# Kernel tuning notes

Hardware: AMD Instinct MI355X
Metric: run time of the kernel (lower is better)

Reference implementation:

```python
import jax, jax.numpy as jnp
import numpy as np

EPS = 1e-8
ALPHA = 0.5


def _min_max_normalize(y):
    y_min = jnp.min(y)
    y_max = jnp.max(y)
    return (y - y_min) / (y_max - y_min + EPS)


def setup_inputs() -> dict:
    key = jax.random.key(0)
    k1, k2, k3, k4 = jax.random.split(key, 4)
    nr, nb, d = 8, 2048, 32
    n_train = 8192
    x = jax.random.uniform(k1, (nr, nb, d), dtype=jnp.float32)
    train_x = jax.random.uniform(k2, (n_train, d), dtype=jnp.float32)
    train_residuals = jax.random.uniform(k3, (n_train,), dtype=jnp.float32)
    sigma_x = jax.random.uniform(k4, (nr, nb), dtype=jnp.float32)
    return {"x": x, "train_x": train_x,
            "train_residuals": train_residuals, "sigma_x": sigma_x}


def reference(x, train_x, train_residuals, sigma_x):
    nr, nb, d = x.shape
    n = train_x.shape[0]

    # Scott's rule bandwidth: mean(std(X, dim=0)) * n^(-1/(d+4)); torch std is unbiased
    std_devs = jnp.std(train_x, axis=0, ddof=1)
    bandwidth = jnp.mean(std_devs) * (float(n) ** (-1.0 / (d + 4)))
    inv_bw_sq = 1.0 / (2.0 * bandwidth * bandwidth)

    # KDE residual estimate (Nadaraya-Watson): cdist^2 -> exp -> weighted sum
    xq = x.reshape(nr * nb, d)                     # [m, d]
    d2 = (jnp.sum(xq * xq, axis=1)[:, None]
          + jnp.sum(train_x * train_x, axis=1)[None, :]
          - 2.0 * (xq @ train_x.T))                # [m, n]
    d2 = jnp.maximum(d2, 0.0)
    kernel_weights = jnp.exp(-d2 * inv_bw_sq)      # [m, n]
    rx = (kernel_weights @ train_residuals) / (jnp.sum(kernel_weights, axis=1) + EPS)

    T1 = ALPHA * _min_max_normalize(rx).reshape(nr, nb)
    T2 = (1.0 - ALPHA) * _min_max_normalize(sigma_x.reshape(-1)).reshape(nr, nb)
    return T1 + T2
```

## Files before the change

kernel.cpp:

```cpp
#include <hip/hip_runtime.h>
#include <math.h>

#define EPSF 1e-8f
#define LOG2E 1.44269504f

typedef short short8 __attribute__((ext_vector_type(8)));
typedef float floatx4 __attribute__((ext_vector_type(4)));

__device__ __forceinline__ unsigned short f2bf(float f) {
    unsigned u = __builtin_bit_cast(unsigned, f);
    unsigned r = (u + 0x7FFFu + ((u >> 16) & 1u)) >> 16;
    return (unsigned short)r;
}
__device__ __forceinline__ float bf2f(unsigned short h) {
    return __builtin_bit_cast(float, ((unsigned)h) << 16);
}

__global__ __launch_bounds__(256) void prep_kernel(const float* __restrict__ x,
                                                   const float* __restrict__ train,
                                                   int n, int m,
                                                   float* __restrict__ tnorm,
                                                   float* __restrict__ qn,
                                                   unsigned short* __restrict__ thi,
                                                   unsigned short* __restrict__ tlo,
                                                   double* __restrict__ pS1,
                                                   double* __restrict__ pS2) {
    int tid = threadIdx.x;
    int b = blockIdx.x;
    if (b < 32) {
        __shared__ double s1s[256];
        __shared__ double s2s[256];
        int rowsPerBlock = n >> 5;
        int rbase = b * rowsPerBlock;
        for (int r = rbase + tid; r < rbase + rowsPerBlock; r += 256) {
            const float4* row = (const float4*)(train + (size_t)r * 32);
            float s = 0.f;
#pragma unroll
            for (int kb = 0; kb < 4; ++kb) {
                float4 f0 = row[kb * 2], f1 = row[kb * 2 + 1];
                float fv[8] = {f0.x, f0.y, f0.z, f0.w, f1.x, f1.y, f1.z, f1.w};
                short8 h, l;
#pragma unroll
                for (int j = 0; j < 8; ++j) {
                    unsigned short hb = f2bf(fv[j]);
                    h[j] = (short)hb;
                    l[j] = (short)f2bf(fv[j] - bf2f(hb));
                    s = fmaf(fv[j], fv[j], s);
                }
                *(short8*)(thi + (size_t)r * 32 + kb * 8) = h;
                *(short8*)(tlo + (size_t)r * 32 + kb * 8) = l;
            }
            tnorm[r] = s;
        }
        int dim = tid & 31;
        int grp = tid >> 5;
        int rpt = rowsPerBlock >> 3;
        int r0 = rbase + grp * rpt;
        double s1 = 0.0, s2 = 0.0;
        for (int i = 0; i < rpt; ++i) {
            float v = train[(size_t)(r0 + i) * 32 + dim];
            s1 += (double)v;
            s2 += (double)v * (double)v;
        }
        s1s[tid] = s1;
        s2s[tid] = s2;
        __syncthreads();
        if (tid < 32) {
            double a = 0.0, c2 = 0.0;
            for (int g = 0; g < 8; ++g) { a += s1s[g * 32 + tid]; c2 += s2s[g * 32 + tid]; }
            pS1[b * 32 + tid] = a;
            pS2[b * 32 + tid] = c2;
        }
    } else {
        int r = (b - 32) * 256 + tid;
        if (r < m) {
            const float4* row = (const float4*)(x + (size_t)r * 32);
            float s = 0.f;
#pragma unroll
            for (int k = 0; k < 8; ++k) {
                float4 t = row[k];
                s = fmaf(t.x, t.x, s); s = fmaf(t.y, t.y, s);
                s = fmaf(t.z, t.z, s); s = fmaf(t.w, t.w, s);
            }
            qn[r] = s;
        }
    }
}

__global__ __launch_bounds__(256, 4) void kde_kernel(const float* __restrict__ x,
                                                     const unsigned short* __restrict__ thi,
                                                     const unsigned short* __restrict__ tlo,
                                                     const float* __restrict__ resid,
                                                     const float* __restrict__ tnorm,
                                                     const float* __restrict__ qn,
                                                     const double* __restrict__ pS1,
                                                     const double* __restrict__ pS2,
                                                     int m, int n, int nchunks,
                                                     float* __restrict__ numP,
                                                     float* __restrict__ denP) {
    __shared__ double sred[32];
    __shared__ float sC[2];
    int tid = threadIdx.x;

    if (tid < 32) {
        double a = 0.0, b2 = 0.0;
        for (int k = 0; k < 32; ++k) { a += pS1[k * 32 + tid]; b2 += pS2[k * 32 + tid]; }
        double var = (b2 - a * a / (double)n) / (double)(n - 1);
        sred[tid] = sqrt(var);
    }
    __syncthreads();
    if (tid == 0) {
        float ms = 0.f;
        for (int k = 0; k < 32; ++k) ms += (float)sred[k];
        ms *= (1.0f / 32.0f);
        float bw = ms * powf((float)n, -1.0f / 36.0f);
        float c = 1.0f / (2.0f * bw * bw);
        sC[0] = -c * LOG2E;
        sC[1] = 2.0f * c * LOG2E;
    }
    __syncthreads();
    float negcl = sC[0], C2 = sC[1];

    int lane = tid & 63;
    int wave = tid >> 6;
    int col = lane & 15;
    int quad = lane >> 4;
    int Mbase = blockIdx.x * 128 + wave * 32;
    int chunk = n / nchunks;
    int Nstart = blockIdx.y * chunk;

    short8 ah[2], al[2];
#pragma unroll
    for (int s = 0; s < 2; ++s) {
        const float* xp = x + (size_t)(Mbase + s * 16 + col) * 32 + quad * 8;
        float4 f0 = *(const float4*)xp;
        float4 f1 = *(const float4*)(xp + 4);
        float fv[8] = {f0.x, f0.y, f0.z, f0.w, f1.x, f1.y, f1.z, f1.w};
#pragma unroll
        for (int j = 0; j < 8; ++j) {
            unsigned short hb = f2bf(fv[j]);
            ah[s][j] = (short)hb;
            al[s][j] = (short)f2bf(fv[j] - bf2f(hb));
        }
    }

    float alpha[2][4];
#pragma unroll
    for (int s = 0; s < 2; ++s)
#pragma unroll
        for (int r = 0; r < 4; ++r)
            alpha[s][r] = negcl * qn[Mbase + s * 16 + quad * 4 + r];

    float num[2][4] = {{0.f, 0.f, 0.f, 0.f}, {0.f, 0.f, 0.f, 0.f}};
    float den[2][4] = {{0.f, 0.f, 0.f, 0.f}, {0.f, 0.f, 0.f, 0.f}};

#pragma unroll 2
    for (int t = 0; t < chunk; t += 16) {
        int row = Nstart + t + col;
        const short8 bh = *(const short8*)(thi + (size_t)row * 32 + quad * 8);
        const short8 bl = *(const short8*)(tlo + (size_t)row * 32 + quad * 8);
        float beta = negcl * tnorm[row];
        float rv = resid[row];

#pragma unroll
        for (int s = 0; s < 2; ++s) {
            floatx4 acc = {0.f, 0.f, 0.f, 0.f};
            acc = __builtin_amdgcn_mfma_f32_16x16x32_bf16(ah[s], bh, acc, 0, 0, 0);
            acc = __builtin_amdgcn_mfma_f32_16x16x32_bf16(ah[s], bl, acc, 0, 0, 0);
            acc = __builtin_amdgcn_mfma_f32_16x16x32_bf16(al[s], bh, acc, 0, 0, 0);
#pragma unroll
            for (int r = 0; r < 4; ++r) {
                float arg = fminf(fmaf(C2, acc[r], alpha[s][r] + beta), 0.0f);
                float w = exp2f(arg);
                num[s][r] = fmaf(w, rv, num[s][r]);
                den[s][r] += w;
            }
        }
    }

#pragma unroll
    for (int s = 0; s < 2; ++s)
#pragma unroll
        for (int r = 0; r < 4; ++r) {
#pragma unroll
            for (int msk = 1; msk < 16; msk <<= 1) {
                num[s][r] += __shfl_xor(num[s][r], msk);
                den[s][r] += __shfl_xor(den[s][r], msk);
            }
        }
    if (col == 0) {
#pragma unroll
        for (int s = 0; s < 2; ++s)
#pragma unroll
            for (int r = 0; r < 4; ++r) {
                int q = Mbase + s * 16 + quad * 4 + r;
                numP[(size_t)blockIdx.y * m + q] = num[s][r];
                denP[(size_t)blockIdx.y * m + q] = den[s][r];
            }
    }
}

__global__ __launch_bounds__(256) void reduce_kernel(const float* __restrict__ numP,
                                                     const float* __restrict__ denP,
                                                     const float* __restrict__ sigma,
                                                     float* __restrict__ rxbuf,
                                                     float* __restrict__ bred,
                                                     int m, int nchunks, int nb) {
    __shared__ float red[256];
    int tid = threadIdx.x;
    int q = blockIdx.x * 256 + tid;

    float num = 0.f, den = 0.f;
    for (int s = 0; s < nchunks; ++s) {
        num += numP[(size_t)s * m + q];
        den += denP[(size_t)s * m + q];
    }
    float rx = num / (den + EPSF);
    rxbuf[q] = rx;
    float sg = sigma[q];

    red[tid] = rx; __syncthreads();
    for (int o = 128; o > 0; o >>= 1) { if (tid < o) red[tid] = fminf(red[tid], red[tid + o]); __syncthreads(); }
    if (tid == 0) bred[0 * nb + blockIdx.x] = red[0];
    __syncthreads();
    red[tid] = rx; __syncthreads();
    for (int o = 128; o > 0; o >>= 1) { if (tid < o) red[tid] = fmaxf(red[tid], red[tid + o]); __syncthreads(); }
    if (tid == 0) bred[1 * nb + blockIdx.x] = red[0];
    __syncthreads();
    red[tid] = sg; __syncthreads();
    for (int o = 128; o > 0; o >>= 1) { if (tid < o) red[tid] = fminf(red[tid], red[tid + o]); __syncthreads(); }
    if (tid == 0) bred[2 * nb + blockIdx.x] = red[0];
    __syncthreads();
    red[tid] = sg; __syncthreads();
    for (int o = 128; o > 0; o >>= 1) { if (tid < o) red[tid] = fmaxf(red[tid], red[tid + o]); __syncthreads(); }
    if (tid == 0) bred[3 * nb + blockIdx.x] = red[0];
}

__global__ __launch_bounds__(256) void combine_kernel(const float* __restrict__ rxbuf,
                                                      const float* __restrict__ sigma,
                                                      const float* __restrict__ bred,
                                                      float* __restrict__ out,
                                                      int m, int nb) {
    __shared__ float sc[4];
    int tid = threadIdx.x;
    if (tid < 64) {
        float v0 = (tid < nb) ? bred[0 * nb + tid] : INFINITY;
        float v1 = (tid < nb) ? bred[1 * nb + tid] : -INFINITY;
        float v2 = (tid < nb) ? bred[2 * nb + tid] : INFINITY;
        float v3 = (tid < nb) ? bred[3 * nb + tid] : -INFINITY;
        for (int o = 32; o > 0; o >>= 1) {
            v0 = fminf(v0, __shfl_xor(v0, o));
            v1 = fmaxf(v1, __shfl_xor(v1, o));
            v2 = fminf(v2, __shfl_xor(v2, o));
            v3 = fmaxf(v3, __shfl_xor(v3, o));
        }
        if (tid == 0) {
            sc[0] = v0;
            sc[1] = 1.0f / (v1 - v0 + EPSF);
            sc[2] = v2;
            sc[3] = 1.0f / (v3 - v2 + EPSF);
        }
    }
    __syncthreads();
    int q = blockIdx.x * 256 + tid;
    if (q >= m) return;
    float t1 = 0.5f * (rxbuf[q] - sc[0]) * sc[1];
    float t2 = 0.5f * (sigma[q] - sc[2]) * sc[3];
    out[q] = t1 + t2;
}

extern "C" void kernel_launch(void* const* d_in, const int* in_sizes, int n_in,
                              void* d_out, int out_size, void* d_ws, size_t ws_size,
                              hipStream_t stream) {
    const float* x     = (const float*)d_in[0];
    const float* train = (const float*)d_in[1];
    const float* resid = (const float*)d_in[2];
    const float* sigma = (const float*)d_in[3];
    float* out = (float*)d_out;

    int n = in_sizes[2];
    int m = in_sizes[3];
    int nb = m / 256;

    double* pS1   = (double*)d_ws;
    double* pS2   = pS1 + 1024;
    float*  tnorm = (float*)(pS2 + 1024);
    float*  qn    = tnorm + n;
    float*  rxbuf = qn + m;
    float*  bred  = rxbuf + m;
    unsigned short* thi = (unsigned short*)(bred + 4 * nb);
    unsigned short* tlo = thi + (size_t)n * 32;
    float* numP = (float*)(tlo + (size_t)n * 32);
    size_t baseBytes = (size_t)((char*)numP - (char*)d_ws);

    int nchunks = 16;
    while (nchunks > 1 &&
           baseBytes + (size_t)2 * nchunks * m * sizeof(float) > ws_size)
        nchunks >>= 1;
    float* denP = numP + (size_t)nchunks * m;

    prep_kernel<<<32 + (m + 255) / 256, 256, 0, stream>>>(x, train, n, m, tnorm, qn,
                                                          thi, tlo, pS1, pS2);

    dim3 grid_c(m / 128, nchunks);
    kde_kernel<<<grid_c, 256, 0, stream>>>(x, thi, tlo, resid, tnorm, qn,
                                           pS1, pS2, m, n, nchunks, numP, denP);

    reduce_kernel<<<nb, 256, 0, stream>>>(numP, denP, sigma, rxbuf, bred, m, nchunks, nb);
    combine_kernel<<<nb, 256, 0, stream>>>(rxbuf, sigma, bred, out, m, nb);
}
```

Baseline: 137.3 us.

## Interleave bf16 hi/lo train data, pack norm+residual, fuse reduce and combine

Stores the hi and lo bf16 halves of each training row interleaved in a single buffer, and packs each row's squared norm with its residual as a float2, so the KDE loop issues fewer, contiguous loads. It also switches to the raw hardware exp2 intrinsic, raises the occupancy hint to 8 blocks, and doubles the N-chunk split to 32. The separate reduce and combine kernels are merged into one, using an atomic counter so the last block finishes normalization, which saves a launch but adds a memset and a serial tail handled by a single block.

New measurement: 181.0 us. +31.8%, slower.

```diff
diff --git a/kernel.cpp b/kernel.cpp
--- a/kernel.cpp
+++ b/kernel.cpp
@@ -18,11 +18,11 @@
 
 __global__ __launch_bounds__(256) void prep_kernel(const float* __restrict__ x,
                                                    const float* __restrict__ train,
+                                                   const float* __restrict__ resid,
                                                    int n, int m,
-                                                   float* __restrict__ tnorm,
+                                                   float2* __restrict__ tr2,
                                                    float* __restrict__ qn,
-                                                   unsigned short* __restrict__ thi,
-                                                   unsigned short* __restrict__ tlo,
+                                                   short* __restrict__ tb,
                                                    double* __restrict__ pS1,
                                                    double* __restrict__ pS2) {
     int tid = threadIdx.x;
@@ -47,10 +47,10 @@
                     l[j] = (short)f2bf(fv[j] - bf2f(hb));
                     s = fmaf(fv[j], fv[j], s);
                 }
-                *(short8*)(thi + (size_t)r * 32 + kb * 8) = h;
-                *(short8*)(tlo + (size_t)r * 32 + kb * 8) = l;
-            }
-            tnorm[r] = s;
+                *(short8*)(tb + (size_t)r * 64 + kb * 16) = h;
+                *(short8*)(tb + (size_t)r * 64 + kb * 16 + 8) = l;
+            }
+            tr2[r] = make_float2(s, resid[r]);
         }
         int dim = tid & 31;
         int grp = tid >> 5;
@@ -87,11 +87,9 @@
     }
 }
 
-__global__ __launch_bounds__(256, 4) void kde_kernel(const float* __restrict__ x,
-                                                     const unsigned short* __restrict__ thi,
-                                                     const unsigned short* __restrict__ tlo,
-                                                     const float* __restrict__ resid,
-                                                     const float* __restrict__ tnorm,
+__global__ __launch_bounds__(256, 8) void kde_kernel(const float* __restrict__ x,
+                                                     const short* __restrict__ tb,
+                                                     const float2* __restrict__ tr2,
                                                      const float* __restrict__ qn,
                                                      const double* __restrict__ pS1,
                                                      const double* __restrict__ pS2,
@@ -128,6 +126,7 @@
     int Mbase = blockIdx.x * 128 + wave * 32;
     int chunk = n / nchunks;
     int Nstart = blockIdx.y * chunk;
+    int ntiles = chunk >> 4;
 
     short8 ah[2], al[2];
 #pragma unroll
@@ -154,13 +153,15 @@
     float num[2][4] = {{0.f, 0.f, 0.f, 0.f}, {0.f, 0.f, 0.f, 0.f}};
     float den[2][4] = {{0.f, 0.f, 0.f, 0.f}, {0.f, 0.f, 0.f, 0.f}};
 
-#pragma unroll 2
-    for (int t = 0; t < chunk; t += 16) {
-        int row = Nstart + t + col;
-        const short8 bh = *(const short8*)(thi + (size_t)row * 32 + quad * 8);
-        const short8 bl = *(const short8*)(tlo + (size_t)row * 32 + quad * 8);
-        float beta = negcl * tnorm[row];
-        float rv = resid[row];
+    const short* tp = tb + (size_t)(Nstart + col) * 64 + quad * 16;
+    const float2* trp = tr2 + Nstart + col;
+
+    for (int it = 0; it < ntiles; ++it) {
+        const short8 bh = *(const short8*)(tp);
+        const short8 bl = *(const short8*)(tp + 8);
+        float2 tv = *trp;
+        float beta = negcl * tv.x;
+        float rv = tv.y;
 
 #pragma unroll
         for (int s = 0; s < 2; ++s) {
@@ -171,11 +172,13 @@
 #pragma unroll
             for (int r = 0; r < 4; ++r) {
                 float arg = fminf(fmaf(C2, acc[r], alpha[s][r] + beta), 0.0f);
-                float w = exp2f(arg);
+                float w = __builtin_amdgcn_exp2f(arg);
                 num[s][r] = fmaf(w, rv, num[s][r]);
                 den[s][r] += w;
             }
         }
+        tp += 16 * 64;
+        trp += 16;
     }
 
 #pragma unroll
@@ -200,12 +203,14 @@
     }
 }
 
-__global__ __launch_bounds__(256) void reduce_kernel(const float* __restrict__ numP,
-                                                     const float* __restrict__ denP,
-                                                     const float* __restrict__ sigma,
-                                                     float* __restrict__ rxbuf,
-                                                     float* __restrict__ bred,
-                                                     int m, int nchunks, int nb) {
+__global__ __launch_bounds__(256) void reduce_combine(const float* __restrict__ numP,
+                                                      const float* __restrict__ denP,
+                                                      const float* __restrict__ sigma,
+                                                      float* __restrict__ rxbuf,
+                                                      float* __restrict__ bred,
+                                                      unsigned* __restrict__ counter,
+                                                      float* __restrict__ out,
+                                                      int m, int nchunks, int nb) {
     __shared__ float red[256];
     int tid = threadIdx.x;
     int q = blockIdx.x * 256 + tid;
@@ -234,15 +239,16 @@
     red[tid] = sg; __syncthreads();
     for (int o = 128; o > 0; o >>= 1) { if (tid < o) red[tid] = fmaxf(red[tid], red[tid + o]); __syncthreads(); }
     if (tid == 0) bred[3 * nb + blockIdx.x] = red[0];
-}
-
-__global__ __launch_bounds__(256) void combine_kernel(const float* __restrict__ rxbuf,
-                                                      const float* __restrict__ sigma,
-                                                      const float* __restrict__ bred,
-                                                      float* __restrict__ out,
-                                                      int m, int nb) {
+
+    __shared__ unsigned done;
+    __threadfence();
+    __syncthreads();
+    if (tid == 0) done = atomicAdd(counter, 1u);
+    __syncthreads();
+    if (done != (unsigned)(nb - 1)) return;
+    __threadfence();
+
     __shared__ float sc[4];
-    int tid = threadIdx.x;
     if (tid < 64) {
         float v0 = (tid < nb) ? bred[0 * nb + tid] : INFINITY;
         float v1 = (tid < nb) ? bred[1 * nb + tid] : -INFINITY;
@@ -262,11 +268,12 @@
         }
     }
     __syncthreads();
-    int q = blockIdx.x * 256 + tid;
-    if (q >= m) return;
-    float t1 = 0.5f * (rxbuf[q] - sc[0]) * sc[1];
-    float t2 = 0.5f * (sigma[q] - sc[2]) * sc[3];
-    out[q] = t1 + t2;
+    float rxmin = sc[0], invr = sc[1], smin = sc[2], invs = sc[3];
+    for (int qq = tid; qq < m; qq += 256) {
+        float t1 = 0.5f * (rxbuf[qq] - rxmin) * invr;
+        float t2 = 0.5f * (sigma[qq] - smin) * invs;
+        out[qq] = t1 + t2;
+    }
 }
 
 extern "C" void kernel_launch(void* const* d_in, const int* in_sizes, int n_in,
@@ -282,30 +289,32 @@
     int m = in_sizes[3];
     int nb = m / 256;
 
-    double* pS1   = (double*)d_ws;
-    double* pS2   = pS1 + 1024;
-    float*  tnorm = (float*)(pS2 + 1024);
-    float*  qn    = tnorm + n;
-    float*  rxbuf = qn + m;
-    float*  bred  = rxbuf + m;
-    unsigned short* thi = (unsigned short*)(bred + 4 * nb);
-    unsigned short* tlo = thi + (size_t)n * 32;
-    float* numP = (float*)(tlo + (size_t)n * 32);
+    double* pS1    = (double*)d_ws;
+    double* pS2    = pS1 + 1024;
+    float2* tr2    = (float2*)(pS2 + 1024);
+    float*  qn     = (float*)(tr2 + n);
+    float*  rxbuf  = qn + m;
+    float*  bred   = rxbuf + m;
+    unsigned* counter = (unsigned*)(bred + 4 * nb);
+    short*  tb     = (short*)(counter + 4);
+    float*  numP   = (float*)(tb + (size_t)n * 64);
     size_t baseBytes = (size_t)((char*)numP - (char*)d_ws);
 
-    int nchunks = 16;
+    int nchunks = 32;
     while (nchunks > 1 &&
            baseBytes + (size_t)2 * nchunks * m * sizeof(float) > ws_size)
         nchunks >>= 1;
     float* denP = numP + (size_t)nchunks * m;
 
-    prep_kernel<<<32 + (m + 255) / 256, 256, 0, stream>>>(x, train, n, m, tnorm, qn,
-                                                          thi, tlo, pS1, pS2);
+    hipMemsetAsync(counter, 0, sizeof(unsigned), stream);
+
+    prep_kernel<<<32 + (m + 255) / 256, 256, 0, stream>>>(x, train, resid, n, m,
+                                                          tr2, qn, tb, pS1, pS2);
 
     dim3 grid_c(m / 128, nchunks);
-    kde_kernel<<<grid_c, 256, 0, stream>>>(x, thi, tlo, resid, tnorm, qn,
-                                           pS1, pS2, m, n, nchunks, numP, denP);
-
-    reduce_kernel<<<nb, 256, 0, stream>>>(numP, denP, sigma, rxbuf, bred, m, nchunks, nb);
-    combine_kernel<<<nb, 256, 0, stream>>>(rxbuf, sigma, bred, out, m, nb);
-}
+    kde_kernel<<<grid_c, 256, 0, stream>>>(x, tb, tr2, qn, pS1, pS2,
+                                           m, n, nchunks, numP, denP);
+
+    reduce_combine<<<nb, 256, 0, stream>>>(numP, denP, sigma, rxbuf, bred,
+                                           counter, out, m, nchunks, nb);
+}
```
